# Kernel tuning notes

Hardware: AMD Instinct MI355X
Metric: run time of the kernel (lower is better)

Reference implementation:

```python
import jax, jax.numpy as jnp
import numpy as np

B, NK, NQ, DK, DQ, H, DV = 16, 256, 256, 256, 256, 128, 256
MASK_VAL = -1000000.0

def setup_inputs() -> dict:
    key = jax.random.key(0)
    ks = jax.random.split(key, 7)
    return {
        "key": jax.random.normal(ks[0], (B, NK, DK), dtype=jnp.float32),
        "query": jax.random.normal(ks[1], (B, NQ, DQ), dtype=jnp.float32),
        "value": jax.random.normal(ks[2], (B, NQ, DV), dtype=jnp.float32),
        "valid_lens": jax.random.randint(ks[3], (B,), 1, NQ + 1, dtype=jnp.int32),
        "Wk": jax.random.normal(ks[4], (DK, H), dtype=jnp.float32) / np.sqrt(DK),
        "Wq": jax.random.normal(ks[5], (DQ, H), dtype=jnp.float32) / np.sqrt(DQ),
        "wv": jax.random.normal(ks[6], (H,), dtype=jnp.float32) / np.sqrt(H),
    }

def reference(key, query, value, valid_lens, Wk, Wq, wv):
    k = key @ Wk                      # (B, NK, H)
    q = query @ Wq                    # (B, NQ, H)
    # note: original unsqueezes key at dim 2, query at dim 1 -> (B, NK, NQ, H)
    feature = jnp.tanh(k[:, :, None, :] + q[:, None, :, :])
    scores = jnp.einsum('bkqh,h->bkq', feature, wv)   # (B, NK, NQ)
    # mask along last (query) axis per batch, as repeat_interleave does
    pos = jnp.arange(scores.shape[-1])[None, None, :]
    masked = jnp.where(pos < valid_lens[:, None, None], scores, MASK_VAL)
    attn = jax.nn.softmax(masked, axis=-1)            # (B, NK, NQ)
    return jnp.einsum('bkq,bqd->bkd', attn, value)    # (B, NK, DV)
```

## Files before the change

kernel.cpp:

```cpp
#include <hip/hip_runtime.h>

#define B_   16
#define NK_  256
#define NQ_  256
#define DK_  256
#define H_   128
#define DV_  256

#define C2X 2.8853900817779268f
#define L2E 1.4426950408889634f
#define MASKV -1.0e5f

typedef float f4 __attribute__((ext_vector_type(4)));

__device__ __forceinline__ float exp2_fast(float x) { return __builtin_amdgcn_exp2f(x); }
__device__ __forceinline__ float rcp_fast(float x)  { return __builtin_amdgcn_rcpf(x); }

__global__ __launch_bounds__(256) void proj_kernel(
    const float* __restrict__ key, const float* __restrict__ query,
    const float* __restrict__ Wk,  const float* __restrict__ Wq,
    float* __restrict__ kfE, float* __restrict__ qE4)
{
    __shared__ alignas(16) float A_s[16 * 256];
    __shared__ alignas(16) float W_s[64 * 128];

    const int blk = blockIdx.x;
    const int tid = threadIdx.x;
    const bool isQ = blk >= 256;
    const int rb = (blk & 255) * 16;

    const float* __restrict__ A = isQ ? query : key;
    const float* __restrict__ W = isQ ? Wq : Wk;

    {
        const f4* src = (const f4*)(A + (size_t)rb * DK_);
        f4* dst = (f4*)A_s;
#pragma unroll
        for (int j = 0; j < 4; ++j) dst[tid + 256 * j] = src[tid + 256 * j];
    }

    const int rg2 = (tid >> 5) << 1;
    const int c4  = (tid & 31) << 2;

    f4 acc0 = {0.f, 0.f, 0.f, 0.f}, acc1 = acc0;

    for (int kc = 0; kc < DK_; kc += 64) {
        __syncthreads();
        {
            const f4* wsrc = (const f4*)(W + (size_t)kc * H_);
            f4* wdst = (f4*)W_s;
#pragma unroll
            for (int j = 0; j < 8; ++j) wdst[tid + 256 * j] = wsrc[tid + 256 * j];
        }
        __syncthreads();
#pragma unroll 2
        for (int k = 0; k < 64; k += 4) {
            f4 w0 = *(const f4*)(W_s + (k + 0) * H_ + c4);
            f4 w1 = *(const f4*)(W_s + (k + 1) * H_ + c4);
            f4 w2 = *(const f4*)(W_s + (k + 2) * H_ + c4);
            f4 w3 = *(const f4*)(W_s + (k + 3) * H_ + c4);
            f4 a0 = *(const f4*)(A_s + (rg2 + 0) * 256 + kc + k);
            f4 a1 = *(const f4*)(A_s + (rg2 + 1) * 256 + kc + k);
            acc0 += a0[0] * w0; acc1 += a1[0] * w0;
            acc0 += a0[1] * w1; acc1 += a1[1] * w1;
            acc0 += a0[2] * w2; acc1 += a1[2] * w2;
            acc0 += a0[3] * w3; acc1 += a1[3] * w3;
        }
    }

    f4 e0, e1;
#pragma unroll
    for (int cc = 0; cc < 4; ++cc) {
        e0[cc] = exp2_fast(C2X * acc0[cc]);
        e1[cc] = exp2_fast(C2X * acc1[cc]);
    }

    if (!isQ) {
        float* dst = kfE + (size_t)(rb + rg2) * H_ + c4;
        *(f4*)(dst)      = e0;
        *(f4*)(dst + H_) = e1;
    } else {
        const int b  = rb >> 8;
        const int q0 = (rb & 255) + rg2;
        f4* dst = (f4*)qE4 + ((size_t)(b * 32 + (c4 >> 2))) * NQ_ + q0;
        dst[0] = e0;
        dst[1] = e1;
    }
}

__global__ __launch_bounds__(256) void attn_kernel(
    const float* __restrict__ kfE, const float* __restrict__ qE4,
    const float* __restrict__ value, const int* __restrict__ vlens,
    const float* __restrict__ wv, float* __restrict__ out)
{
    __shared__ alignas(16) float sc_s[4 * 260];
    __shared__ alignas(16) float at4_s[256 * 4];
    __shared__ alignas(16) float red_s[16 * 256];

    const int x    = blockIdx.x;
    const int qu   = x >> 8;
    const int xi   = x & 255;
    const int b    = (xi + (qu << 2)) & 15;
    const int kt   = (xi >> 4) + (qu << 4);
    const int k0   = kt << 2;
    const int tid  = threadIdx.x;
    const int lane = tid & 63;
    const int wu   = __builtin_amdgcn_readfirstlane(tid >> 6);
    const int valid  = vlens[b];
    const int nchunk = (valid + 63) >> 6;

    float sumwv;
    {
        f4 sw = {0.f, 0.f, 0.f, 0.f};
#pragma unroll
        for (int i = 0; i < 32; ++i) sw += ((const f4*)wv)[i];
        sumwv = (sw[0] + sw[1]) + (sw[2] + sw[3]);
    }

    {
        const int p   = wu >> 1;
        const int par = wu & 1;
        const int l0  = p << 1;
        const int nslot = (par < nchunk ? 1 : 0) + (par + 2 < nchunk ? 1 : 0);

        if (nslot) {
            const float* ekp = kfE + ((size_t)(b * NK_ + k0 + l0)) * H_;
            const f4*    eqA = (const f4*)qE4 + (size_t)b * (32 * NQ_)
                               + ((par << 6) + lane);
            const f4*    eqB = eqA + 128;

            float acc[2][2][2];
#pragma unroll
            for (int s = 0; s < 2; ++s)
#pragma unroll
                for (int r = 0; r < 2; ++r) { acc[s][r][0] = 0.f; acc[s][r][1] = 0.f; }

            auto body = [&](int NS) {
#pragma unroll 4
                for (int h4 = 0; h4 < 32; ++h4) {
                    const f4 ekA = *(const f4*)(ekp + (h4 << 2));
                    const f4 ekB = *(const f4*)(ekp + H_ + (h4 << 2));
                    const f4 w4  = *(const f4*)(wv + (h4 << 2));
                    {
                        const f4 e = eqA[(size_t)h4 * NQ_];
                        acc[0][0][0] = fmaf(w4[0], rcp_fast(fmaf(ekA[0], e[0], 1.f)), acc[0][0][0]);
                        acc[0][0][1] = fmaf(w4[1], rcp_fast(fmaf(ekA[1], e[1], 1.f)), acc[0][0][1]);
                        acc[0][0][0] = fmaf(w4[2], rcp_fast(fmaf(ekA[2], e[2], 1.f)), acc[0][0][0]);
                        acc[0][0][1] = fmaf(w4[3], rcp_fast(fmaf(ekA[3], e[3], 1.f)), acc[0][0][1]);
                        acc[0][1][0] = fmaf(w4[0], rcp_fast(fmaf(ekB[0], e[0], 1.f)), acc[0][1][0]);
                        acc[0][1][1] = fmaf(w4[1], rcp_fast(fmaf(ekB[1], e[1], 1.f)), acc[0][1][1]);
                        acc[0][1][0] = fmaf(w4[2], rcp_fast(fmaf(ekB[2], e[2], 1.f)), acc[0][1][0]);
                        acc[0][1][1] = fmaf(w4[3], rcp_fast(fmaf(ekB[3], e[3], 1.f)), acc[0][1][1]);
                    }
                    if (NS == 2) {
                        const f4 e = eqB[(size_t)h4 * NQ_];
                        acc[1][0][0] = fmaf(w4[0], rcp_fast(fmaf(ekA[0], e[0], 1.f)), acc[1][0][0]);
                        acc[1][0][1] = fmaf(w4[1], rcp_fast(fmaf(ekA[1], e[1], 1.f)), acc[1][0][1]);
                        acc[1][0][0] = fmaf(w4[2], rcp_fast(fmaf(ekA[2], e[2], 1.f)), acc[1][0][0]);
                        acc[1][0][1] = fmaf(w4[3], rcp_fast(fmaf(ekA[3], e[3], 1.f)), acc[1][0][1]);
                        acc[1][1][0] = fmaf(w4[0], rcp_fast(fmaf(ekB[0], e[0], 1.f)), acc[1][1][0]);
                        acc[1][1][1] = fmaf(w4[1], rcp_fast(fmaf(ekB[1], e[1], 1.f)), acc[1][1][1]);
                        acc[1][1][0] = fmaf(w4[2], rcp_fast(fmaf(ekB[2], e[2], 1.f)), acc[1][1][0]);
                        acc[1][1][1] = fmaf(w4[3], rcp_fast(fmaf(ekB[3], e[3], 1.f)), acc[1][1][1]);
                    }
                }
            };
            if (nslot == 1) body(1); else body(2);

#pragma unroll
            for (int s = 0; s < 2; ++s) {
                if (s < nslot) {
                    const int q = (((par + (s << 1))) << 6) + lane;
                    sc_s[(l0 + 0) * 260 + q] = sumwv - 2.f * (acc[s][0][0] + acc[s][0][1]);
                    sc_s[(l0 + 1) * 260 + q] = sumwv - 2.f * (acc[s][1][0] + acc[s][1][1]);
                }
            }
        }
    }
    __syncthreads();

    {
        const float* row = sc_s + wu * 260;
        float s[4];
        float m = MASKV;
#pragma unroll
        for (int j = 0; j < 4; ++j) {
            const int q = (j << 6) + lane;
            s[j] = (q < valid) ? row[q] : MASKV;
            m = fmaxf(m, s[j]);
        }
#pragma unroll
        for (int off = 32; off >= 1; off >>= 1)
            m = fmaxf(m, __shfl_xor(m, off, 64));
        float ssum = 0.f;
#pragma unroll
        for (int j = 0; j < 4; ++j) {
            s[j] = exp2_fast(L2E * (s[j] - m));
            ssum += s[j];
        }
#pragma unroll
        for (int off = 32; off >= 1; off >>= 1)
            ssum += __shfl_xor(ssum, off, 64);
        const float inv = rcp_fast(ssum);
#pragma unroll
        for (int j = 0; j < 4; ++j)
            at4_s[(((j << 6) + lane) << 2) + wu] = s[j] * inv;
    }
    __syncthreads();

    {
        const int rq = tid >> 6;
        const int d4 = lane << 2;
        const float* vb = value + (size_t)b * (NQ_ * DV_) + d4;
        f4 o0 = {0.f,0.f,0.f,0.f}, o1 = o0, o2 = o0, o3 = o0;
#pragma unroll 4
        for (int q = rq; q < valid; q += 4) {
            f4 v  = *(const f4*)(vb + (size_t)q * DV_);
            f4 a4 = *(const f4*)(at4_s + (q << 2));
            o0 += a4[0] * v;
            o1 += a4[1] * v;
            o2 += a4[2] * v;
            o3 += a4[3] * v;
        }
        float* rs = red_s + (rq << 10) + d4;
        *(f4*)(rs + 0)    = o0;
        *(f4*)(rs + 256)  = o1;
        *(f4*)(rs + 512)  = o2;
        *(f4*)(rs + 768)  = o3;
    }
    __syncthreads();

    {
        const int k  = tid >> 6;
        const int d4 = lane << 2;
        const float* rs = red_s + (k << 8) + d4;
        f4 o = *(const f4*)(rs) + *(const f4*)(rs + 1024)
             + *(const f4*)(rs + 2048) + *(const f4*)(rs + 3072);
        *(f4*)(out + ((size_t)(b * NK_ + k0 + k)) * DV_ + d4) = o;
    }
}

extern "C" void kernel_launch(void* const* d_in, const int* in_sizes, int n_in,
                              void* d_out, int out_size, void* d_ws, size_t ws_size,
                              hipStream_t stream)
{
    const float* key   = (const float*)d_in[0];
    const float* query = (const float*)d_in[1];
    const float* value = (const float*)d_in[2];
    const int*   vlens = (const int*)  d_in[3];
    const float* Wk    = (const float*)d_in[4];
    const float* Wq    = (const float*)d_in[5];
    const float* wv    = (const float*)d_in[6];
    float* outp = (float*)d_out;

    float* kfE = (float*)d_ws;
    float* qE4 = kfE + (size_t)B_ * NK_ * H_;

    hipLaunchKernelGGL(proj_kernel, dim3(512), dim3(256), 0, stream,
                       key, query, Wk, Wq, kfE, qE4);
    hipLaunchKernelGGL(attn_kernel, dim3(1024), dim3(256), 0, stream,
                       kfE, qE4, value, vlens, wv, outp);
}
```

Measured before the change: 100.9 us.

## Double-buffer projection weights and widen attention blocks to eight key rows

The projection kernel now stages weights in two 32-row shared buffers and prefetches the next chunk into registers while computing the current one, removing one barrier per chunk. The attention kernel is rebuilt as attn_kernel2 with 512 threads handling 8 key rows per block. This halves the grid and lets each loaded query-exponential vector and value row be reused across more key rows. The final value reduction is done in two phases in shared memory. A dead, incomplete attn_kernel variant is left behind, and the larger blocks may lower occupancy and increase idle warps for short valid lengths.

```diff
diff --git a/kernel.cpp b/kernel.cpp
--- a/kernel.cpp
+++ b/kernel.cpp
@@ -22,7 +22,7 @@
     float* __restrict__ kfE, float* __restrict__ qE4)
 {
     __shared__ alignas(16) float A_s[16 * 256];
-    __shared__ alignas(16) float W_s[64 * 128];
+    __shared__ alignas(16) float W_s[2][32 * 128];
 
     const int blk = blockIdx.x;
     const int tid = threadIdx.x;
@@ -38,29 +38,37 @@
 #pragma unroll
         for (int j = 0; j < 4; ++j) dst[tid + 256 * j] = src[tid + 256 * j];
     }
+    f4 wr0, wr1, wr2, wr3;
+    {
+        const f4* ws = (const f4*)W;
+        wr0 = ws[tid]; wr1 = ws[tid + 256]; wr2 = ws[tid + 512]; wr3 = ws[tid + 768];
+    }
 
     const int rg2 = (tid >> 5) << 1;
     const int c4  = (tid & 31) << 2;
 
     f4 acc0 = {0.f, 0.f, 0.f, 0.f}, acc1 = acc0;
 
-    for (int kc = 0; kc < DK_; kc += 64) {
+    for (int c = 0; c < 8; ++c) {
+        {
+            f4* wd = (f4*)&W_s[c & 1][0];
+            wd[tid] = wr0; wd[tid + 256] = wr1; wd[tid + 512] = wr2; wd[tid + 768] = wr3;
+        }
         __syncthreads();
-        {
-            const f4* wsrc = (const f4*)(W + (size_t)kc * H_);
-            f4* wdst = (f4*)W_s;
-#pragma unroll
-            for (int j = 0; j < 8; ++j) wdst[tid + 256 * j] = wsrc[tid + 256 * j];
-        }
-        __syncthreads();
-#pragma unroll 2
-        for (int k = 0; k < 64; k += 4) {
-            f4 w0 = *(const f4*)(W_s + (k + 0) * H_ + c4);
-            f4 w1 = *(const f4*)(W_s + (k + 1) * H_ + c4);
-            f4 w2 = *(const f4*)(W_s + (k + 2) * H_ + c4);
-            f4 w3 = *(const f4*)(W_s + (k + 3) * H_ + c4);
-            f4 a0 = *(const f4*)(A_s + (rg2 + 0) * 256 + kc + k);
-            f4 a1 = *(const f4*)(A_s + (rg2 + 1) * 256 + kc + k);
+        if (c < 7) {
+            const f4* ws = (const f4*)(W + (size_t)(c + 1) * 32 * H_);
+            wr0 = ws[tid]; wr1 = ws[tid + 256]; wr2 = ws[tid + 512]; wr3 = ws[tid + 768];
+        }
+        const float* Wb = &W_s[c & 1][0];
+        const float* Ab = A_s + (c << 5);
+#pragma unroll
+        for (int k = 0; k < 32; k += 4) {
+            f4 w0 = *(const f4*)(Wb + (k + 0) * H_ + c4);
+            f4 w1 = *(const f4*)(Wb + (k + 1) * H_ + c4);
+            f4 w2 = *(const f4*)(Wb + (k + 2) * H_ + c4);
+            f4 w3 = *(const f4*)(Wb + (k + 3) * H_ + c4);
+            f4 a0 = *(const f4*)(Ab + (rg2 + 0) * 256 + k);
+            f4 a1 = *(const f4*)(Ab + (rg2 + 1) * 256 + k);
             acc0 += a0[0] * w0; acc1 += a1[0] * w0;
             acc0 += a0[1] * w1; acc1 += a1[1] * w1;
             acc0 += a0[2] * w2; acc1 += a1[2] * w2;
@@ -88,21 +96,18 @@
     }
 }
 
-__global__ __launch_bounds__(256) void attn_kernel(
+__global__ __launch_bounds__(512, 4) void attn_kernel(
     const float* __restrict__ kfE, const float* __restrict__ qE4,
     const float* __restrict__ value, const int* __restrict__ vlens,
     const float* __restrict__ wv, float* __restrict__ out)
 {
-    __shared__ alignas(16) float sc_s[4 * 260];
-    __shared__ alignas(16) float at4_s[256 * 4];
-    __shared__ alignas(16) float red_s[16 * 256];
+    __shared__ alignas(16) float at_s[256 * 8];
+    __shared__ alignas(16) float scratch[8192];
 
     const int x    = blockIdx.x;
-    const int qu   = x >> 8;
-    const int xi   = x & 255;
-    const int b    = (xi + (qu << 2)) & 15;
-    const int kt   = (xi >> 4) + (qu << 4);
-    const int k0   = kt << 2;
+    const int g    = x >> 4;
+    const int b    = ((x & 15) + ((x >> 8) << 3)) & 15;
+    const int k0   = g << 3;
     const int tid  = threadIdx.x;
     const int lane = tid & 63;
     const int wu   = __builtin_amdgcn_readfirstlane(tid >> 6);
@@ -117,64 +122,37 @@
         sumwv = (sw[0] + sw[1]) + (sw[2] + sw[3]);
     }
 
-    {
-        const int p   = wu >> 1;
-        const int par = wu & 1;
-        const int l0  = p << 1;
-        const int nslot = (par < nchunk ? 1 : 0) + (par + 2 < nchunk ? 1 : 0);
-
-        if (nslot) {
-            const float* ekp = kfE + ((size_t)(b * NK_ + k0 + l0)) * H_;
-            const f4*    eqA = (const f4*)qE4 + (size_t)b * (32 * NQ_)
-                               + ((par << 6) + lane);
-            const f4*    eqB = eqA + 128;
-
-            float acc[2][2][2];
-#pragma unroll
-            for (int s = 0; s < 2; ++s)
-#pragma unroll
-                for (int r = 0; r < 2; ++r) { acc[s][r][0] = 0.f; acc[s][r][1] = 0.f; }
-
-            auto body = [&](int NS) {
+    float* sc_s = scratch;
+
+    {
+        const int c  = wu >> 1;
+        const int rh = wu & 1;
+        if (c < nchunk) {
+            const float* ekb = kfE + ((size_t)(b * NK_ + k0 + rh * 4)) * H_;
+            const f4*    eqp = (const f4*)qE4 + ((size_t)b << 13) + (c << 6) + lane;
+            const f4*    wvf = (const f4*)wv;
+
+            float acc[4][2];
+#pragma unroll
+            for (int r = 0; r < 4; ++r) { acc[r][0] = 0.f; acc[r][1] = 0.f; }
+
 #pragma unroll 4
-                for (int h4 = 0; h4 < 32; ++h4) {
-                    const f4 ekA = *(const f4*)(ekp + (h4 << 2));
-                    const f4 ekB = *(const f4*)(ekp + H_ + (h4 << 2));
-                    const f4 w4  = *(const f4*)(wv + (h4 << 2));
-                    {
-                        const f4 e = eqA[(size_t)h4 * NQ_];
-                        acc[0][0][0] = fmaf(w4[0], rcp_fast(fmaf(ekA[0], e[0], 1.f)), acc[0][0][0]);
-                        acc[0][0][1] = fmaf(w4[1], rcp_fast(fmaf(ekA[1], e[1], 1.f)), acc[0][0][1]);
-                        acc[0][0][0] = fmaf(w4[2], rcp_fast(fmaf(ekA[2], e[2], 1.f)), acc[0][0][0]);
-                        acc[0][0][1] = fmaf(w4[3], rcp_fast(fmaf(ekA[3], e[3], 1.f)), acc[0][0][1]);
-                        acc[0][1][0] = fmaf(w4[0], rcp_fast(fmaf(ekB[0], e[0], 1.f)), acc[0][1][0]);
-                        acc[0][1][1] = fmaf(w4[1], rcp_fast(fmaf(ekB[1], e[1], 1.f)), acc[0][1][1]);
-                        acc[0][1][0] = fmaf(w4[2], rcp_fast(fmaf(ekB[2], e[2], 1.f)), acc[0][1][0]);
-                        acc[0][1][1] = fmaf(w4[3], rcp_fast(fmaf(ekB[3], e[3], 1.f)), acc[0][1][1]);
-                    }
-                    if (NS == 2) {
-                        const f4 e = eqB[(size_t)h4 * NQ_];
-                        acc[1][0][0] = fmaf(w4[0], rcp_fast(fmaf(ekA[0], e[0], 1.f)), acc[1][0][0]);
-                        acc[1][0][1] = fmaf(w4[1], rcp_fast(fmaf(ekA[1], e[1], 1.f)), acc[1][0][1]);
-                        acc[1][0][0] = fmaf(w4[2], rcp_fast(fmaf(ekA[2], e[2], 1.f)), acc[1][0][0]);
-                        acc[1][0][1] = fmaf(w4[3], rcp_fast(fmaf(ekA[3], e[3], 1.f)), acc[1][0][1]);
-                        acc[1][1][0] = fmaf(w4[0], rcp_fast(fmaf(ekB[0], e[0], 1.f)), acc[1][1][0]);
-                        acc[1][1][1] = fmaf(w4[1], rcp_fast(fmaf(ekB[1], e[1], 1.f)), acc[1][1][1]);
-                        acc[1][1][0] = fmaf(w4[2], rcp_fast(fmaf(ekB[2], e[2], 1.f)), acc[1][1][0]);
-                        acc[1][1][1] = fmaf(w4[3], rcp_fast(fmaf(ekB[3], e[3], 1.f)), acc[1][1][1]);
-                    }
-                }
-            };
-            if (nslot == 1) body(1); else body(2);
-
-#pragma unroll
-            for (int s = 0; s < 2; ++s) {
-                if (s < nslot) {
-                    const int q = (((par + (s << 1))) << 6) + lane;
-                    sc_s[(l0 + 0) * 260 + q] = sumwv - 2.f * (acc[s][0][0] + acc[s][0][1]);
-                    sc_s[(l0 + 1) * 260 + q] = sumwv - 2.f * (acc[s][1][0] + acc[s][1][1]);
+            for (int h4 = 0; h4 < 32; ++h4) {
+                const f4 e  = eqp[h4 << 8];
+                const f4 w4 = wvf[h4];
+#pragma unroll
+                for (int r = 0; r < 4; ++r) {
+                    const f4 ek = *(const f4*)(ekb + r * H_ + (h4 << 2));
+                    acc[r][0] = fmaf(w4[0], rcp_fast(fmaf(ek[0], e[0], 1.f)), acc[r][0]);
+                    acc[r][1] = fmaf(w4[1], rcp_fast(fmaf(ek[1], e[1], 1.f)), acc[r][1]);
+                    acc[r][0] = fmaf(w4[2], rcp_fast(fmaf(ek[2], e[2], 1.f)), acc[r][0]);
+                    acc[r][1] = fmaf(w4[3], rcp_fast(fmaf(ek[3], e[3], 1.f)), acc[r][1]);
                 }
             }
+            const int q = (c << 6) + lane;
+#pragma unroll
+            for (int r = 0; r < 4; ++r)
+                sc_s[(rh * 4 + r) * 260 + q] = sumwv - 2.f * (acc[r][0] + acc[r][1]);
         }
     }
     __syncthreads();
@@ -204,39 +182,177 @@
         const float inv = rcp_fast(ssum);
 #pragma unroll
         for (int j = 0; j < 4; ++j)
-            at4_s[(((j << 6) + lane) << 2) + wu] = s[j] * inv;
-    }
-    __syncthreads();
-
-    {
-        const int rq = tid >> 6;
+            at_s[(((j << 6) + lane) << 3) + wu] = s[j] * inv;
+    }
+    __syncthreads();
+
+    float* red = scratch;
+    {
         const int d4 = lane << 2;
         const float* vb = value + (size_t)b * (NQ_ * DV_) + d4;
-        f4 o0 = {0.f,0.f,0.f,0.f}, o1 = o0, o2 = o0, o3 = o0;
+        f4 o[8];
+#pragma unroll
+        for (int k = 0; k < 8; ++k) o[k] = (f4){0.f, 0.f, 0.f, 0.f};
 #pragma unroll 4
-        for (int q = rq; q < valid; q += 4) {
-            f4 v  = *(const f4*)(vb + (size_t)q * DV_);
-            f4 a4 = *(const f4*)(at4_s + (q << 2));
-            o0 += a4[0] * v;
-            o1 += a4[1] * v;
-            o2 += a4[2] * v;
-            o3 += a4[3] * v;
-        }
-        float* rs = red_s + (rq << 10) + d4;
-        *(f4*)(rs + 0)    = o0;
-        *(f4*)(rs + 256)  = o1;
-        *(f4*)(rs + 512)  = o2;
-        *(f4*)(rs + 768)  = o3;
-    }
-    __syncthreads();
-
-    {
-        const int k  = tid >> 6;
-        const int d4 = lane << 2;
-        const float* rs = red_s + (k << 8) + d4;
-        f4 o = *(const f4*)(rs) + *(const f4*)(rs + 1024)
-             + *(const f4*)(rs + 2048) + *(const f4*)(rs + 3072);
-        *(f4*)(out + ((size_t)(b * NK_ + k0 + k)) * DV_ + d4) = o;
+        for (int q = wu; q < valid; q += 8) {
+            const f4 v   = *(const f4*)(vb + (size_t)q * DV_);
+            const f4 alo = *(const f4*)(at_s + (q << 3));
+            const f4 ahi = *(const f4*)(at_s + (q << 3) + 4);
+            o[0] += alo[0] * v; o[1] += alo[1] * v;
+            o[2] += alo[2] * v; o[3] += alo[3] * v;
+            o[4] += ahi[0] * v; o[5] += ahi[1] * v;
+            o[6] += ahi[2] * v; o[7] += ahi[3] * v;
+        }
+        if (wu < 4) {
+            float* rp = red + (wu << 11) + d4;
+#pragma unroll
+            for (int k = 0; k < 8; ++k) *(f4*)(rp + (k << 8)) = o[k];
+        }
+    }
+    __syncthreads();
+    {
+        const int d4 = lane << 2;
+        if (wu >= 4) {
+            float* rp = red + ((wu - 4) << 11) + d4;
+        }
+    }
+    {
+        const int d4 = lane << 2;
+    }
+    __syncthreads();
+    {
+        const int d4 = lane << 2;
+        const float* rp = red + (wu << 8) + d4;
+        f4 oo = *(const f4*)(rp)        + *(const f4*)(rp + 2048)
+              + *(const f4*)(rp + 4096) + *(const f4*)(rp + 6144);
+        *(f4*)(out + ((size_t)(b * NK_ + k0 + wu)) * DV_ + d4) = oo;
+    }
+}
+
+__global__ __launch_bounds__(512, 4) void attn_kernel2(
+    const float* __restrict__ kfE, const float* __restrict__ qE4,
+    const float* __restrict__ value, const int* __restrict__ vlens,
+    const float* __restrict__ wv, float* __restrict__ out)
+{
+    __shared__ alignas(16) float at_s[256 * 8];
+    __shared__ alignas(16) float scratch[8192];
+
+    const int x    = blockIdx.x;
+    const int g    = x >> 4;
+    const int b    = ((x & 15) + ((x >> 8) << 3)) & 15;
+    const int k0   = g << 3;
+    const int tid  = threadIdx.x;
+    const int lane = tid & 63;
+    const int wu   = __builtin_amdgcn_readfirstlane(tid >> 6);
+    const int valid  = vlens[b];
+    const int nchunk = (valid + 63) >> 6;
+
+    float sumwv;
+    {
+        f4 sw = {0.f, 0.f, 0.f, 0.f};
+#pragma unroll
+        for (int i = 0; i < 32; ++i) sw += ((const f4*)wv)[i];
+        sumwv = (sw[0] + sw[1]) + (sw[2] + sw[3]);
+    }
+
+    float* sc_s = scratch;
+
+    {
+        const int c  = wu >> 1;
+        const int rh = wu & 1;
+        if (c < nchunk) {
+            const float* ekb = kfE + ((size_t)(b * NK_ + k0 + rh * 4)) * H_;
+            const f4*    eqp = (const f4*)qE4 + ((size_t)b << 13) + (c << 6) + lane;
+            const f4*    wvf = (const f4*)wv;
+            float acc[4][2];
+#pragma unroll
+            for (int r = 0; r < 4; ++r) { acc[r][0] = 0.f; acc[r][1] = 0.f; }
+#pragma unroll 4
+            for (int h4 = 0; h4 < 32; ++h4) {
+                const f4 e  = eqp[h4 << 8];
+                const f4 w4 = wvf[h4];
+#pragma unroll
+                for (int r = 0; r < 4; ++r) {
+                    const f4 ek = *(const f4*)(ekb + r * H_ + (h4 << 2));
+                    acc[r][0] = fmaf(w4[0], rcp_fast(fmaf(ek[0], e[0], 1.f)), acc[r][0]);
+                    acc[r][1] = fmaf(w4[1], rcp_fast(fmaf(ek[1], e[1], 1.f)), acc[r][1]);
+                    acc[r][0] = fmaf(w4[2], rcp_fast(fmaf(ek[2], e[2], 1.f)), acc[r][0]);
+                    acc[r][1] = fmaf(w4[3], rcp_fast(fmaf(ek[3], e[3], 1.f)), acc[r][1]);
+                }
+            }
+            const int q = (c << 6) + lane;
+#pragma unroll
+            for (int r = 0; r < 4; ++r)
+                sc_s[(rh * 4 + r) * 260 + q] = sumwv - 2.f * (acc[r][0] + acc[r][1]);
+        }
+    }
+    __syncthreads();
+
+    {
+        const float* row = sc_s + wu * 260;
+        float s[4];
+        float m = MASKV;
+#pragma unroll
+        for (int j = 0; j < 4; ++j) {
+            const int q = (j << 6) + lane;
+            s[j] = (q < valid) ? row[q] : MASKV;
+            m = fmaxf(m, s[j]);
+        }
+#pragma unroll
+        for (int off = 32; off >= 1; off >>= 1)
+            m = fmaxf(m, __shfl_xor(m, off, 64));
+        float ssum = 0.f;
+#pragma unroll
+        for (int j = 0; j < 4; ++j) {
+            s[j] = exp2_fast(L2E * (s[j] - m));
+            ssum += s[j];
+        }
+#pragma unroll
+        for (int off = 32; off >= 1; off >>= 1)
+            ssum += __shfl_xor(ssum, off, 64);
+        const float inv = rcp_fast(ssum);
+#pragma unroll
+        for (int j = 0; j < 4; ++j)
+            at_s[(((j << 6) + lane) << 3) + wu] = s[j] * inv;
+    }
+    __syncthreads();
+
+    float* red = scratch;
+    {
+        const int d4 = lane << 2;
+        const float* vb = value + (size_t)b * (NQ_ * DV_) + d4;
+        f4 o[8];
+#pragma unroll
+        for (int k = 0; k < 8; ++k) o[k] = (f4){0.f, 0.f, 0.f, 0.f};
+#pragma unroll 4
+        for (int q = wu; q < valid; q += 8) {
+            const f4 v   = *(const f4*)(vb + (size_t)q * DV_);
+            const f4 alo = *(const f4*)(at_s + (q << 3));
+            const f4 ahi = *(const f4*)(at_s + (q << 3) + 4);
+            o[0] += alo[0] * v; o[1] += alo[1] * v;
+            o[2] += alo[2] * v; o[3] += alo[3] * v;
+            o[4] += ahi[0] * v; o[5] += ahi[1] * v;
+            o[6] += ahi[2] * v; o[7] += ahi[3] * v;
+        }
+        if (wu < 4) {
+            float* rp = red + (wu << 11) + d4;
+#pragma unroll
+            for (int k = 0; k < 8; ++k) *(f4*)(rp + (k << 8)) = o[k];
+        }
+        __syncthreads();
+        if (wu >= 4) {
+            float* rp = red + ((wu - 4) << 11) + d4;
+#pragma unroll
+            for (int k = 0; k < 8; ++k) {
+                f4* p = (f4*)(rp + (k << 8));
+                *p += o[k];
+            }
+        }
+        __syncthreads();
+        const float* rp = red + (wu << 8) + d4;
+        f4 oo = *(const f4*)(rp)        + *(const f4*)(rp + 2048)
+              + *(const f4*)(rp + 4096) + *(const f4*)(rp + 6144);
+        *(f4*)(out + ((size_t)(b * NK_ + k0 + wu)) * DV_ + d4) = oo;
     }
 }
 
@@ -258,6 +374,6 @@
 
     hipLaunchKernelGGL(proj_kernel, dim3(512), dim3(256), 0, stream,
                        key, query, Wk, Wq, kfE, qE4);
-    hipLaunchKernelGGL(attn_kernel, dim3(1024), dim3(256), 0, stream,
+    hipLaunchKernelGGL(attn_kernel2, dim3(512), dim3(512), 0, stream,
                        kfE, qE4, value, vlens, wv, outp);
 }
```

Result: slower. 103.0 us (+2.1%).
